# Kernel tuning notes

Measured on AMD Instinct MI355X. Metric: run time of the kernel, lower is better.

Reference implementation:

```python
import jax, jax.numpy as jnp
import numpy as np

K = 3            # char conv window (in words of chars)
B, P, LC = 64, 80, 18   # batch, padded sentence len, padded word char len
E = 256          # embedding_dim (shared by word and char embeddings)
H = 1024         # lstm hidden
L_CH = 4         # conv output channels
VOCAB, ALPHA, TAGS = 50000, 100, 50


def setup_inputs() -> dict:
    key = jax.random.key(0)
    ks = jax.random.split(key, 12)
    D = E + L_CH  # lstm input dim
    s = 0.02
    return {
        "sentence_batch": jax.random.randint(ks[0], (B, P), 0, VOCAB),
        "character_batch": jax.random.randint(ks[1], (B, P, LC), 0, ALPHA),
        "word_emb": jax.random.normal(ks[2], (VOCAB, E), jnp.float32) * s,
        "char_emb": jax.random.normal(ks[3], (ALPHA, E), jnp.float32) * s,
        "conv_w": jax.random.normal(ks[4], (L_CH, K * E), jnp.float32) * s,
        "conv_b": jax.random.normal(ks[5], (L_CH,), jnp.float32) * s,
        "w_ih": jax.random.normal(ks[6], (4 * H, D), jnp.float32) * s,
        "w_hh": jax.random.normal(ks[7], (4 * H, H), jnp.float32) * s,
        "b_ih": jax.random.normal(ks[8], (4 * H,), jnp.float32) * s,
        "b_hh": jax.random.normal(ks[9], (4 * H,), jnp.float32) * s,
        "out_w": jax.random.normal(ks[10], (TAGS, H), jnp.float32) * s,
        "out_b": jax.random.normal(ks[11], (TAGS,), jnp.float32) * s,
    }


def reference(sentence_batch, character_batch, word_emb, char_emb, conv_w,
              conv_b, w_ih, w_hh, b_ih, b_hh, out_w, out_b):
    # --- char CNN: sliding K-window over char embeddings, flatten, linear, max ---
    ce = char_emb[character_batch]                      # [B,P,LC,E]
    Wn = LC - K + 1                                     # windows per word
    widx = jnp.arange(Wn)[:, None] + jnp.arange(K)      # [Wn,K]
    win = ce[:, :, widx, :].reshape(B, P, Wn, K * E)    # [B,P,Wn,K*E]
    # Conv1d(in=1, out=4, kernel=K*E) on a length-K*E input == one linear per window
    phi = jnp.einsum('bpwd,cd->bpwc', win, conv_w) + conv_b  # [B,P,Wn,4]
    char_repr = phi.max(axis=2)                         # [B,P,4] (max over windows)

    # --- word embeddings + concat ---
    we = word_emb[sentence_batch]                       # [B,P,E]
    combined = jnp.concatenate([we, char_repr], axis=2) # [B,P,E+4]
    D = combined.shape[-1]
    # faithful to torch: .view(PADDING_SIZE, BATCH_SIZE, -1) is a reshape, not transpose
    x = combined.reshape(P, B, D)                       # [P,B,D]

    # --- LSTM (torch gate order i,f,g,o) ---
    def step(carry, x_t):
        h, c = carry
        gates = x_t @ w_ih.T + b_ih + h @ w_hh.T + b_hh  # [B,4H]
        i, f, g, o = jnp.split(gates, 4, axis=-1)
        i = jax.nn.sigmoid(i)
        f = jax.nn.sigmoid(f)
        g = jnp.tanh(g)
        o = jax.nn.sigmoid(o)
        c = f * c + i * g
        h = o * jnp.tanh(c)
        return (h, c), h

    h0 = jnp.zeros((B, H), x.dtype)
    c0 = jnp.zeros((B, H), x.dtype)
    _, hs = jax.lax.scan(step, (h0, c0), x)             # [P,B,H]

    # faithful reshape back, linear head, log_softmax over dim=1 (the P axis)
    lstm_out = hs.reshape(B, P, H)
    tag_space = lstm_out @ out_w.T + out_b              # [B,P,TAGS]
    return jax.nn.log_softmax(tag_space, axis=1)
```

## Files before the change

kernel.cpp:

```cpp
#include <hip/hip_runtime.h>
#include <math.h>

#define BB 64
#define PP 80
#define LC 18
#define EE 256
#define HH 1024
#define LCH 4
#define KW 3
#define TAGS 50
#define DD 260
#define KPAD 288
#define ROWS (BB*PP)
#define WN (LC-KW+1)
#define NG (4*HH)
#define GRP 4
#define NBLK (GRP*64)
#define HSTEP (GRP*32*512)

typedef __attribute__((ext_vector_type(8))) short short8;
typedef __attribute__((ext_vector_type(4))) short short4v;
typedef __attribute__((ext_vector_type(4))) float floatx4;
typedef __attribute__((ext_vector_type(4))) int int4v;

__device__ __forceinline__ short f2bf(float x) {
    unsigned u = __float_as_uint(x);
    unsigned r = (u + 0x7FFFu + ((u >> 16) & 1u)) >> 16;
    return (short)r;
}
__device__ __forceinline__ float bf2f(short s) {
    return __uint_as_float(((unsigned)(unsigned short)s) << 16);
}
__device__ __forceinline__ float sigf(float x) { return 1.f / (1.f + __expf(-x)); }
__device__ __forceinline__ float tanhfast(float x) {
    float e = __expf(2.f * x);
    return 1.f - 2.f / (e + 1.f);
}
__device__ __forceinline__ float wave_reduce_sum(float v) {
    for (int off = 32; off > 0; off >>= 1) v += __shfl_xor(v, off, 64);
    return v;
}

__global__ __launch_bounds__(256) void prep_kernel(
    const float* __restrict__ wih, const float* __restrict__ whh,
    const float* __restrict__ outw,
    short* __restrict__ wih_bf, short* __restrict__ wpk,
    short* __restrict__ outw_bf, unsigned* __restrict__ flags)
{
    const int NI = NG * KPAD;
    const int NH = NG * HH;
    const int NO = 64 * HH;
    const int total = NI + NH + NO;
    for (int i = blockIdx.x * 256 + threadIdx.x; i < total; i += gridDim.x * 256) {
        if (i < NI) {
            int r = i / KPAD, c = i - r * KPAD;
            wih_bf[i] = (c < DD) ? f2bf(wih[r * DD + c]) : (short)0;
        } else if (i < NI + NH) {
            int o = i - NI;
            int e  = o & 7;
            int l  = (o >> 3) & 63;
            int s  = (o >> 9) & 3;
            int tl = (o >> 11) & 3;
            int w  = (o >> 13) & 7;
            int bl = o >> 16;
            int row = tl * HH + bl * 16 + (l & 15);
            int col = w * 128 + s * 32 + (l >> 4) * 8 + e;
            wpk[o] = f2bf(whh[(size_t)row * HH + col]);
        } else {
            int k = i - NI - NH;
            int r = k >> 10;
            outw_bf[k] = (r < TAGS) ? f2bf(outw[k]) : (short)0;
        }
    }
    for (int i = blockIdx.x * 256 + threadIdx.x; i < PP * GRP * 64; i += gridDim.x * 256)
        flags[i] = 0u;
}

__global__ __launch_bounds__(256) void embed_kernel(
    const int* __restrict__ sent, const int* __restrict__ chars,
    const float* __restrict__ word_emb, const float* __restrict__ char_emb,
    const float* __restrict__ conv_w, const float* __restrict__ conv_b,
    short* __restrict__ X)
{
    __shared__ float4 ce[LC * 64];
    __shared__ float phi[WN * LCH];
    __shared__ float charrep[LCH];
    const int r = blockIdx.x;
    const int t = threadIdx.x;
    const int lane = t & 63, wv = t >> 6;

    const int cbase = r * LC;
    for (int i = 0; i < 5; ++i) {
        int idx = i * 256 + t;
        if (idx < LC * 64) {
            int j = idx >> 6, e4 = idx & 63;
            int ch = chars[cbase + j];
            ce[idx] = ((const float4*)(char_emb + (size_t)ch * EE))[e4];
        }
    }
    float4 cw[KW][LCH];
    #pragma unroll
    for (int k = 0; k < KW; ++k)
        #pragma unroll
        for (int c = 0; c < LCH; ++c)
            cw[k][c] = ((const float4*)(conv_w + c * (KW * EE) + k * EE))[lane];
    __syncthreads();

    #pragma unroll
    for (int wi = 0; wi < 4; ++wi) {
        int w = wv + wi * 4;
        float acc[LCH] = {0.f, 0.f, 0.f, 0.f};
        #pragma unroll
        for (int k = 0; k < KW; ++k) {
            float4 v = ce[(w + k) * 64 + lane];
            #pragma unroll
            for (int c = 0; c < LCH; ++c)
                acc[c] += v.x * cw[k][c].x + v.y * cw[k][c].y +
                          v.z * cw[k][c].z + v.w * cw[k][c].w;
        }
        #pragma unroll
        for (int c = 0; c < LCH; ++c) {
            float s = wave_reduce_sum(acc[c]);
            if (lane == 0) phi[w * LCH + c] = s;
        }
    }
    __syncthreads();
    if (t < LCH) {
        float m = -1e30f;
        for (int w = 0; w < WN; ++w) m = fmaxf(m, phi[w * LCH + t]);
        charrep[t] = m + conv_b[t];
    }
    __syncthreads();

    const int word = sent[r];
    X[(size_t)r * KPAD + t] = f2bf(word_emb[(size_t)word * EE + t]);
    if (t < LCH) X[(size_t)r * KPAD + EE + t] = f2bf(charrep[t]);
    if (t >= 228) X[(size_t)r * KPAD + 32 + t] = (short)0;
}

__global__ __launch_bounds__(256) void gemm_in_kernel(
    const short* __restrict__ X, const short* __restrict__ Wih,
    const float* __restrict__ b_ih, const float* __restrict__ b_hh,
    short* __restrict__ ginP)
{
    const int tid = threadIdx.x;
    const int l = tid & 63, wv = tid >> 6;
    const int r0 = blockIdx.x * 64;
    const int n0 = blockIdx.y * 128 + wv * 32;
    const int lr = l & 15, lh = l >> 4;

    floatx4 acc[4][2];
    #pragma unroll
    for (int m = 0; m < 4; ++m)
        #pragma unroll
        for (int n = 0; n < 2; ++n) acc[m][n] = (floatx4)0.f;

    const short* Xb = X + (size_t)(r0 + lr) * KPAD + lh * 8;
    const short* Wb = Wih + (size_t)(n0 + lr) * KPAD + lh * 8;

    #pragma unroll
    for (int k0 = 0; k0 < KPAD; k0 += 32) {
        short8 a0 = *(const short8*)(Xb + k0);
        short8 a1 = *(const short8*)(Xb + 16 * KPAD + k0);
        short8 a2 = *(const short8*)(Xb + 32 * KPAD + k0);
        short8 a3 = *(const short8*)(Xb + 48 * KPAD + k0);
        short8 b0 = *(const short8*)(Wb + k0);
        short8 b1 = *(const short8*)(Wb + 16 * KPAD + k0);
        acc[0][0] = __builtin_amdgcn_mfma_f32_16x16x32_bf16(a0, b0, acc[0][0], 0, 0, 0);
        acc[1][0] = __builtin_amdgcn_mfma_f32_16x16x32_bf16(a1, b0, acc[1][0], 0, 0, 0);
        acc[2][0] = __builtin_amdgcn_mfma_f32_16x16x32_bf16(a2, b0, acc[2][0], 0, 0, 0);
        acc[3][0] = __builtin_amdgcn_mfma_f32_16x16x32_bf16(a3, b0, acc[3][0], 0, 0, 0);
        acc[0][1] = __builtin_amdgcn_mfma_f32_16x16x32_bf16(a0, b1, acc[0][1], 0, 0, 0);
        acc[1][1] = __builtin_amdgcn_mfma_f32_16x16x32_bf16(a1, b1, acc[1][1], 0, 0, 0);
        acc[2][1] = __builtin_amdgcn_mfma_f32_16x16x32_bf16(a2, b1, acc[2][1], 0, 0, 0);
        acc[3][1] = __builtin_amdgcn_mfma_f32_16x16x32_bf16(a3, b1, acc[3][1], 0, 0, 0);
    }
    #pragma unroll
    for (int m = 0; m < 4; ++m)
        #pragma unroll
        for (int n = 0; n < 2; ++n) {
            int col = n0 + n * 16 + lr;
            float bias = b_ih[col] + b_hh[col];
            short4v pack;
            #pragma unroll
            for (int q = 0; q < 4; ++q) pack[q] = f2bf(acc[m][n][q] + bias);
            int w_ = col >> 10, bl_ = (col >> 4) & 63, uu_ = col & 15;
            size_t addr = ((((size_t)(blockIdx.x * GRP + m) * 64 + bl_) * 4 + w_) * 16
                           + uu_) * 16 + lh * 4;
            *(short4v*)(ginP + addr) = pack;
        }
}

__global__ __launch_bounds__(512, 1) void lstm_seq_kernel(
    short* __restrict__ hst, const short* __restrict__ wpk,
    const short* __restrict__ ginP, unsigned* __restrict__ flags)
{
    __shared__ __align__(16) float lds_g[8][4][16][20];
    __shared__ short8 hbufv[16][2];

    const int tid = threadIdx.x;
    const int l = tid & 63;
    const int w = tid >> 6;
    const int g  = blockIdx.x >> 6;
    const int bl = blockIdx.x & 63;

    short8 barr[4][4];
    {
        const short* wb = wpk + ((size_t)(bl * 8 + w) * 16) * 512 + l * 8;
        #pragma unroll
        for (int tl = 0; tl < 4; ++tl)
            #pragma unroll
            for (int s = 0; s < 4; ++s)
                barr[tl][s] = *(const short8*)(wb + (tl * 4 + s) * 512);
    }

    const int b16 = tid & 15;
    const int uu  = (tid >> 4) & 15;
    float c = 0.f;

    float gv[4] = {0.f, 0.f, 0.f, 0.f};
    if (tid < 256) {
        const short* gb = ginP + (((size_t)g * 64 + bl) * 4) * 256 + uu * 16 + b16;
        #pragma unroll
        for (int q = 0; q < 4; ++q) gv[q] = bf2f(gb[q * 256]);
    }

    for (int t = 0; t < PP; ++t) {
        if (t > 0) {
            if (tid >= 64 && tid < 128) {
                const unsigned* fl = flags + ((size_t)(t - 1) * GRP + g) * 64;
                while (__hip_atomic_load(fl + (tid - 64), __ATOMIC_RELAXED,
                                         __HIP_MEMORY_SCOPE_AGENT) == 0u)
                    __builtin_amdgcn_s_sleep(1);
            }
            __syncthreads();

            const short* A = hst + (size_t)(t - 1) * HSTEP + g * 16384
                             + (w * 4) * 512 + l * 8;
            int4v a[4];
            #pragma unroll
            for (int s = 0; s < 4; ++s)
                asm volatile("global_load_dwordx4 %0, %1, off sc0 sc1"
                             : "=v"(a[s]) : "v"(A + s * 512) : "memory");
            asm volatile("s_waitcnt vmcnt(0)" ::: "memory");
            __builtin_amdgcn_sched_barrier(0);

            floatx4 acc[4];
            #pragma unroll
            for (int tl = 0; tl < 4; ++tl) acc[tl] = (floatx4)0.f;
            #pragma unroll
            for (int s = 0; s < 4; ++s) {
                short8 av = __builtin_bit_cast(short8, a[s]);
                #pragma unroll
                for (int tl = 0; tl < 4; ++tl)
                    acc[tl] = __builtin_amdgcn_mfma_f32_16x16x32_bf16(
                        av, barr[tl][s], acc[tl], 0, 0, 0);
            }
            #pragma unroll
            for (int tl = 0; tl < 4; ++tl)
                *(floatx4*)&lds_g[w][tl][l & 15][(l >> 4) * 4] = acc[tl];
            __syncthreads();
        }

        if (tid < 256) {
            float s0 = gv[0], s1 = gv[1], s2 = gv[2], s3 = gv[3];
            if (t > 0) {
                #pragma unroll
                for (int w2 = 0; w2 < 8; ++w2) {
                    s0 += lds_g[w2][0][uu][b16];
                    s1 += lds_g[w2][1][uu][b16];
                    s2 += lds_g[w2][2][uu][b16];
                    s3 += lds_g[w2][3][uu][b16];
                }
            }
            float i_ = sigf(s0), f_ = sigf(s1), g_ = tanhfast(s2), o_ = sigf(s3);
            c = f_ * c + i_ * g_;
            ((short*)&hbufv[b16][0])[uu] = f2bf(o_ * tanhfast(c));

            if (t + 1 < PP) {
                const short* gb = ginP + (((size_t)(t + 1) * GRP + g) * 64 + bl) * 1024
                                  + uu * 16 + b16;
                #pragma unroll
                for (int q = 0; q < 4; ++q) gv[q] = bf2f(gb[q * 256]);
            }
        }
        __syncthreads();

        if (tid < 32) {
            int lh8 = tid >> 4, bb = tid & 15;
            int4v hv = __builtin_bit_cast(int4v, hbufv[bb][lh8]);
            int lt = ((2 * bl + lh8) & 3) * 16 + bb;
            short* hp = hst + (size_t)t * HSTEP + g * 16384 + (bl >> 1) * 512 + lt * 8;
            asm volatile("global_store_dwordx4 %0, %1, off sc0 sc1"
                         :: "v"(hp), "v"(hv) : "memory");
        }
        if (t + 1 < PP && w == 0) {
            asm volatile("s_waitcnt vmcnt(0)" ::: "memory");
            if (tid == 0)
                __hip_atomic_store(flags + ((size_t)t * GRP + g) * 64 + bl, 1u,
                                   __ATOMIC_RELAXED, __HIP_MEMORY_SCOPE_AGENT);
        }
    }
}

__global__ __launch_bounds__(256) void tag_kernel(
    const short* __restrict__ hst, const short* __restrict__ outw_bf,
    const float* __restrict__ out_b, float* __restrict__ out)
{
    const int tid = threadIdx.x;
    const int l = tid & 63, wv = tid >> 6;
    const int t = blockIdx.x;
    const int n0 = wv * 16;
    const int lr = l & 15, lh = l >> 4;

    const short* At = hst + (size_t)t * HSTEP;
    const short* Bw = outw_bf + (size_t)(n0 + lr) * HH + lh * 8;

    floatx4 acc[4];
    #pragma unroll
    for (int m = 0; m < 4; ++m) acc[m] = (floatx4)0.f;

    #pragma unroll 4
    for (int kk = 0; kk < 32; ++kk) {
        short8 b = *(const short8*)(Bw + kk * 32);
        #pragma unroll
        for (int m = 0; m < 4; ++m) {
            short8 a = *(const short8*)(At + m * 16384 + kk * 512 + l * 8);
            acc[m] = __builtin_amdgcn_mfma_f32_16x16x32_bf16(a, b, acc[m], 0, 0, 0);
        }
    }
    int col = n0 + lr;
    if (col < TAGS) {
        float bias = out_b[col];
        #pragma unroll
        for (int m = 0; m < 4; ++m)
            #pragma unroll
            for (int q = 0; q < 4; ++q) {
                int row = t * 64 + m * 16 + lh * 4 + q;
                out[(size_t)row * TAGS + col] = acc[m][q] + bias;
            }
    }
}

__global__ __launch_bounds__(256) void logsoftmax_kernel(float* __restrict__ out)
{
    const int tid = threadIdx.x;
    const int lane = tid & 63;
    const int pair = blockIdx.x * 4 + (tid >> 6);
    if (pair >= BB * TAGS) return;
    const int bb = pair / TAGS, g = pair % TAGS;
    float* base = out + (size_t)bb * PP * TAGS + g;
    float v0 = base[lane * TAGS];
    float v1 = (lane < PP - 64) ? base[(lane + 64) * TAGS] : -1e30f;
    float m = fmaxf(v0, v1);
    for (int off = 32; off > 0; off >>= 1) m = fmaxf(m, __shfl_xor(m, off, 64));
    float s = __expf(v0 - m) + ((lane < PP - 64) ? __expf(v1 - m) : 0.f);
    s = wave_reduce_sum(s);
    float lz = m + __logf(s);
    base[lane * TAGS] = v0 - lz;
    if (lane < PP - 64) base[(lane + 64) * TAGS] = v1 - lz;
}

extern "C" void kernel_launch(void* const* d_in, const int* in_sizes, int n_in,
                              void* d_out, int out_size, void* d_ws, size_t ws_size,
                              hipStream_t stream)
{
    const int*   sent     = (const int*)d_in[0];
    const int*   chars    = (const int*)d_in[1];
    const float* word_emb = (const float*)d_in[2];
    const float* char_emb = (const float*)d_in[3];
    const float* conv_w   = (const float*)d_in[4];
    const float* conv_b   = (const float*)d_in[5];
    const float* w_ih     = (const float*)d_in[6];
    const float* w_hh     = (const float*)d_in[7];
    const float* b_ih     = (const float*)d_in[8];
    const float* b_hh     = (const float*)d_in[9];
    const float* out_w    = (const float*)d_in[10];
    const float* out_b    = (const float*)d_in[11];
    float* out = (float*)d_out;

    short* X_bf    = (short*)d_ws;
    short* wih_bf  = X_bf + (size_t)ROWS * KPAD;
    short* wpk     = wih_bf + (size_t)NG * KPAD;
    short* outw_bf = wpk + (size_t)NG * HH;
    short* ginP    = outw_bf + (size_t)64 * HH;
    short* hst     = ginP + (size_t)NG * ROWS;
    unsigned* flags = (unsigned*)(hst + (size_t)PP * HSTEP);

    hipLaunchKernelGGL(prep_kernel, dim3(2048), dim3(256), 0, stream,
                       w_ih, w_hh, out_w, wih_bf, wpk, outw_bf, flags);
    hipLaunchKernelGGL(embed_kernel, dim3(ROWS), dim3(256), 0, stream,
                       sent, chars, word_emb, char_emb, conv_w, conv_b, X_bf);
    hipLaunchKernelGGL(gemm_in_kernel, dim3(ROWS / 64, NG / 128), dim3(256), 0, stream,
                       X_bf, wih_bf, b_ih, b_hh, ginP);
    {
        void* kargs[4] = { (void*)&hst, (void*)&wpk, (void*)&ginP, (void*)&flags };
        hipLaunchCooperativeKernel((void*)lstm_seq_kernel, dim3(NBLK), dim3(512),
                                   kargs, 0, stream);
    }
    hipLaunchKernelGGL(tag_kernel, dim3(PP), dim3(256), 0, stream,
                       hst, outw_bf, out_b, out);
    hipLaunchKernelGGL(logsoftmax_kernel, dim3((BB * TAGS + 3) / 4), dim3(256), 0, stream,
                       out);
}
```

Measured before the change: 485.9 us.

## Replace per-step flag handshake with step-tagged hidden-state words polled directly

Drops the separate flag array and its release store. Each bf16 hidden value is now packed into a 32-bit word together with its timestep tag. Consumer blocks repeatedly load the hidden state and check the tags until every word matches the current step, so the data arrival itself acts as the synchronization. This removes one round-trip (wait for store, set flag, poll flag, then load data) per step. In exchange the hidden-state traffic doubles, the whole hst buffer must be zeroed up front in prep, and the tag kernel has to unpack the words.

```diff
diff --git a/kernel.cpp b/kernel.cpp
--- a/kernel.cpp
+++ b/kernel.cpp
@@ -16,7 +16,7 @@
 #define NG (4*HH)
 #define GRP 4
 #define NBLK (GRP*64)
-#define HSTEP (GRP*32*512)
+#define HSTEP32 (GRP*32*512)
 
 typedef __attribute__((ext_vector_type(8))) short short8;
 typedef __attribute__((ext_vector_type(4))) short short4v;
@@ -45,7 +45,7 @@
     const float* __restrict__ wih, const float* __restrict__ whh,
     const float* __restrict__ outw,
     short* __restrict__ wih_bf, short* __restrict__ wpk,
-    short* __restrict__ outw_bf, unsigned* __restrict__ flags)
+    short* __restrict__ outw_bf, unsigned* __restrict__ hst32)
 {
     const int NI = NG * KPAD;
     const int NH = NG * HH;
@@ -72,8 +72,11 @@
             outw_bf[k] = (r < TAGS) ? f2bf(outw[k]) : (short)0;
         }
     }
-    for (int i = blockIdx.x * 256 + threadIdx.x; i < PP * GRP * 64; i += gridDim.x * 256)
-        flags[i] = 0u;
+    int4v z = {0, 0, 0, 0};
+    int4v* hz = (int4v*)hst32;
+    const int NZ = PP * HSTEP32 / 4;
+    for (int i = blockIdx.x * 256 + threadIdx.x; i < NZ; i += gridDim.x * 256)
+        hz[i] = z;
 }
 
 __global__ __launch_bounds__(256) void embed_kernel(
@@ -192,11 +195,11 @@
 }
 
 __global__ __launch_bounds__(512, 1) void lstm_seq_kernel(
-    short* __restrict__ hst, const short* __restrict__ wpk,
-    const short* __restrict__ ginP, unsigned* __restrict__ flags)
+    unsigned* __restrict__ hst, const short* __restrict__ wpk,
+    const short* __restrict__ ginP)
 {
     __shared__ __align__(16) float lds_g[8][4][16][20];
-    __shared__ short8 hbufv[16][2];
+    __shared__ __align__(16) unsigned hbuf32[16][20];
 
     const int tid = threadIdx.x;
     const int l = tid & 63;
@@ -218,6 +221,11 @@
     const int uu  = (tid >> 4) & 15;
     float c = 0.f;
 
+    const int seg = w * 8 + (l & 7);
+    const int s_lr = seg & 15, s_hl = (seg >> 4) & 1, s_eh = seg >> 5;
+    const int s_ll = (2 * (bl & 1) + s_hl) * 16 + s_lr;
+    const size_t s_off = (size_t)g * 16384 + (size_t)(bl >> 1) * 512 + s_ll * 8 + s_eh * 4;
+
     float gv[4] = {0.f, 0.f, 0.f, 0.f};
     if (tid < 256) {
         const short* gb = ginP + (((size_t)g * 64 + bl) * 4) * 256 + uu * 16 + b16;
@@ -227,30 +235,41 @@
 
     for (int t = 0; t < PP; ++t) {
         if (t > 0) {
-            if (tid >= 64 && tid < 128) {
-                const unsigned* fl = flags + ((size_t)(t - 1) * GRP + g) * 64;
-                while (__hip_atomic_load(fl + (tid - 64), __ATOMIC_RELAXED,
-                                         __HIP_MEMORY_SCOPE_AGENT) == 0u)
-                    __builtin_amdgcn_s_sleep(1);
-            }
-            __syncthreads();
-
-            const short* A = hst + (size_t)(t - 1) * HSTEP + g * 16384
-                             + (w * 4) * 512 + l * 8;
-            int4v a[4];
-            #pragma unroll
-            for (int s = 0; s < 4; ++s)
-                asm volatile("global_load_dwordx4 %0, %1, off sc0 sc1"
-                             : "=v"(a[s]) : "v"(A + s * 512) : "memory");
-            asm volatile("s_waitcnt vmcnt(0)" ::: "memory");
-            __builtin_amdgcn_sched_barrier(0);
+            const unsigned* A = hst + (size_t)(t - 1) * HSTEP32 + g * 16384
+                                + (w * 4) * 512 + l * 8;
+            int4v d[8];
+            int ok;
+            do {
+                #pragma unroll
+                for (int s = 0; s < 4; ++s) {
+                    asm volatile("global_load_dwordx4 %0, %1, off sc0 sc1"
+                                 : "=v"(d[2 * s]) : "v"(A + s * 512) : "memory");
+                    asm volatile("global_load_dwordx4 %0, %1, off sc0 sc1"
+                                 : "=v"(d[2 * s + 1]) : "v"(A + s * 512 + 4) : "memory");
+                }
+                asm volatile("s_waitcnt vmcnt(0)" ::: "memory");
+                __builtin_amdgcn_sched_barrier(0);
+                ok = 1;
+                #pragma unroll
+                for (int i = 0; i < 8; ++i)
+                    #pragma unroll
+                    for (int j = 0; j < 4; ++j)
+                        ok &= ((((unsigned)d[i][j]) & 0xFFFFu) == (unsigned)t);
+                ok = __all(ok);
+                if (!ok) __builtin_amdgcn_s_sleep(2);
+            } while (!ok);
 
             floatx4 acc[4];
             #pragma unroll
             for (int tl = 0; tl < 4; ++tl) acc[tl] = (floatx4)0.f;
             #pragma unroll
             for (int s = 0; s < 4; ++s) {
-                short8 av = __builtin_bit_cast(short8, a[s]);
+                int4v pk;
+                pk[0] = (int)((((unsigned)d[2*s][0]) >> 16)   | (((unsigned)d[2*s][1])   & 0xFFFF0000u));
+                pk[1] = (int)((((unsigned)d[2*s][2]) >> 16)   | (((unsigned)d[2*s][3])   & 0xFFFF0000u));
+                pk[2] = (int)((((unsigned)d[2*s+1][0]) >> 16) | (((unsigned)d[2*s+1][1]) & 0xFFFF0000u));
+                pk[3] = (int)((((unsigned)d[2*s+1][2]) >> 16) | (((unsigned)d[2*s+1][3]) & 0xFFFF0000u));
+                short8 av = __builtin_bit_cast(short8, pk);
                 #pragma unroll
                 for (int tl = 0; tl < 4; ++tl)
                     acc[tl] = __builtin_amdgcn_mfma_f32_16x16x32_bf16(
@@ -275,7 +294,9 @@
             }
             float i_ = sigf(s0), f_ = sigf(s1), g_ = tanhfast(s2), o_ = sigf(s3);
             c = f_ * c + i_ * g_;
-            ((short*)&hbufv[b16][0])[uu] = f2bf(o_ * tanhfast(c));
+            unsigned hd = (((unsigned)(unsigned short)f2bf(o_ * tanhfast(c))) << 16)
+                          | (unsigned)(t + 1);
+            hbuf32[b16][uu] = hd;
 
             if (t + 1 < PP) {
                 const short* gb = ginP + (((size_t)(t + 1) * GRP + g) * 64 + bl) * 1024
@@ -286,25 +307,17 @@
         }
         __syncthreads();
 
-        if (tid < 32) {
-            int lh8 = tid >> 4, bb = tid & 15;
-            int4v hv = __builtin_bit_cast(int4v, hbufv[bb][lh8]);
-            int lt = ((2 * bl + lh8) & 3) * 16 + bb;
-            short* hp = hst + (size_t)t * HSTEP + g * 16384 + (bl >> 1) * 512 + lt * 8;
+        if ((l & 56) == 0) {
+            int4v hv = *(const int4v*)&hbuf32[s_lr][s_hl * 8 + s_eh * 4];
+            unsigned* hp = hst + (size_t)t * HSTEP32 + s_off;
             asm volatile("global_store_dwordx4 %0, %1, off sc0 sc1"
                          :: "v"(hp), "v"(hv) : "memory");
         }
-        if (t + 1 < PP && w == 0) {
-            asm volatile("s_waitcnt vmcnt(0)" ::: "memory");
-            if (tid == 0)
-                __hip_atomic_store(flags + ((size_t)t * GRP + g) * 64 + bl, 1u,
-                                   __ATOMIC_RELAXED, __HIP_MEMORY_SCOPE_AGENT);
-        }
     }
 }
 
 __global__ __launch_bounds__(256) void tag_kernel(
-    const short* __restrict__ hst, const short* __restrict__ outw_bf,
+    const unsigned* __restrict__ hst, const short* __restrict__ outw_bf,
     const float* __restrict__ out_b, float* __restrict__ out)
 {
     const int tid = threadIdx.x;
@@ -313,7 +326,7 @@
     const int n0 = wv * 16;
     const int lr = l & 15, lh = l >> 4;
 
-    const short* At = hst + (size_t)t * HSTEP;
+    const unsigned* At = hst + (size_t)t * HSTEP32;
     const short* Bw = outw_bf + (size_t)(n0 + lr) * HH + lh * 8;
 
     floatx4 acc[4];
@@ -325,7 +338,15 @@
         short8 b = *(const short8*)(Bw + kk * 32);
         #pragma unroll
         for (int m = 0; m < 4; ++m) {
-            short8 a = *(const short8*)(At + m * 16384 + kk * 512 + l * 8);
+            const unsigned* ap = At + m * 16384 + kk * 512 + l * 8;
+            int4v d0 = *(const int4v*)(ap);
+            int4v d1 = *(const int4v*)(ap + 4);
+            int4v pk;
+            pk[0] = (int)((((unsigned)d0[0]) >> 16) | (((unsigned)d0[1]) & 0xFFFF0000u));
+            pk[1] = (int)((((unsigned)d0[2]) >> 16) | (((unsigned)d0[3]) & 0xFFFF0000u));
+            pk[2] = (int)((((unsigned)d1[0]) >> 16) | (((unsigned)d1[1]) & 0xFFFF0000u));
+            pk[3] = (int)((((unsigned)d1[2]) >> 16) | (((unsigned)d1[3]) & 0xFFFF0000u));
+            short8 a = __builtin_bit_cast(short8, pk);
             acc[m] = __builtin_amdgcn_mfma_f32_16x16x32_bf16(a, b, acc[m], 0, 0, 0);
         }
     }
@@ -379,27 +400,26 @@
     const float* out_b    = (const float*)d_in[11];
     float* out = (float*)d_out;
 
-    short* X_bf    = (short*)d_ws;
-    short* wih_bf  = X_bf + (size_t)ROWS * KPAD;
-    short* wpk     = wih_bf + (size_t)NG * KPAD;
-    short* outw_bf = wpk + (size_t)NG * HH;
-    short* ginP    = outw_bf + (size_t)64 * HH;
-    short* hst     = ginP + (size_t)NG * ROWS;
-    unsigned* flags = (unsigned*)(hst + (size_t)PP * HSTEP);
+    short* X_bf     = (short*)d_ws;
+    short* wih_bf   = X_bf + (size_t)ROWS * KPAD;
+    short* wpk      = wih_bf + (size_t)NG * KPAD;
+    short* outw_bf  = wpk + (size_t)NG * HH;
+    short* ginP     = outw_bf + (size_t)64 * HH;
+    unsigned* hst32 = (unsigned*)(ginP + (size_t)NG * ROWS);
 
     hipLaunchKernelGGL(prep_kernel, dim3(2048), dim3(256), 0, stream,
-                       w_ih, w_hh, out_w, wih_bf, wpk, outw_bf, flags);
+                       w_ih, w_hh, out_w, wih_bf, wpk, outw_bf, hst32);
     hipLaunchKernelGGL(embed_kernel, dim3(ROWS), dim3(256), 0, stream,
                        sent, chars, word_emb, char_emb, conv_w, conv_b, X_bf);
     hipLaunchKernelGGL(gemm_in_kernel, dim3(ROWS / 64, NG / 128), dim3(256), 0, stream,
                        X_bf, wih_bf, b_ih, b_hh, ginP);
     {
-        void* kargs[4] = { (void*)&hst, (void*)&wpk, (void*)&ginP, (void*)&flags };
+        void* kargs[3] = { (void*)&hst32, (void*)&wpk, (void*)&ginP };
         hipLaunchCooperativeKernel((void*)lstm_seq_kernel, dim3(NBLK), dim3(512),
                                    kargs, 0, stream);
     }
     hipLaunchKernelGGL(tag_kernel, dim3(PP), dim3(256), 0, stream,
-                       hst, outw_bf, out_b, out);
+                       hst32, outw_bf, out_b, out);
     hipLaunchKernelGGL(logsoftmax_kernel, dim3((BB * TAGS + 3) / 4), dim3(256), 0, stream,
                        out);
 }
```

New measurement: 458.4 us. -5.7%, faster.
